# Performance work log

Measured on AMD Instinct MI355X. Metric: run time of the kernel, lower is better.

## Reference

```python
import jax, jax.numpy as jnp
import numpy as np

NUM_QUESTION = 10000


def setup_inputs() -> dict:
    key = jax.random.key(0)
    ks = jax.random.split(key, 12)
    B, L, DK, SLOTS = 64, 200, 128, 64
    return {
        "question_seq": jax.random.randint(ks[0], (B, L), 0, NUM_QUESTION),
        "correct_seq": jax.random.randint(ks[1], (B, L), 0, 2),
        "q_emb": jax.random.normal(ks[2], (NUM_QUESTION, DK), jnp.float32) * 0.05,
        "v_emb": jax.random.normal(ks[3], (2 * NUM_QUESTION, DK), jnp.float32) * 0.05,
        "Mk": jax.random.normal(ks[4], (SLOTS, DK), jnp.float32) * 0.1,
        "Mv0": jax.random.normal(ks[5], (SLOTS, DK), jnp.float32) * 0.1,
        "eW": jax.random.normal(ks[6], (DK, DK), jnp.float32) * 0.05,
        "eb": jnp.zeros((DK,), jnp.float32),
        "aW": jax.random.normal(ks[7], (DK, DK), jnp.float32) * 0.05,
        "ab": jnp.zeros((DK,), jnp.float32),
        "fW": jax.random.normal(ks[8], (DK, 2 * DK), jnp.float32) * 0.05,
        "fb": jnp.zeros((DK,), jnp.float32),
        "pW": jax.random.normal(ks[9], (1, DK), jnp.float32) * 0.05,
        "pb": jnp.zeros((1,), jnp.float32),
    }


def reference(question_seq, correct_seq, q_emb, v_emb, Mk, Mv0,
              eW, eb, aW, ab, fW, fb, pW, pb):
    B = question_seq.shape[0]
    x = question_seq + NUM_QUESTION * correct_seq          # [B, L]
    k = q_emb[question_seq]                                # [B, L, DK]
    v = v_emb[x]                                           # [B, L, DK]
    w = jax.nn.softmax(jnp.einsum("bld,sd->bls", k, Mk), axis=-1)  # [B, L, S]
    e = jax.nn.sigmoid(v @ eW.T + eb)                      # [B, L, DK]
    a = jnp.tanh(v @ aW.T + ab)                            # [B, L, DK]

    Mv_init = jnp.broadcast_to(Mv0[None], (B,) + Mv0.shape)  # [B, S, DK]

    def step(Mvt, inp):
        wt, et, at = inp  # [B,S], [B,DK], [B,DK]
        # read uses memory BEFORE the write (Mv[:, :-1] in the original)
        read = jnp.einsum("bs,bsd->bd", wt, Mvt)
        we = wt[:, :, None]
        Mvt = Mvt * (1.0 - we * et[:, None, :]) + we * at[:, None, :]
        return Mvt, read

    xs = (w.transpose(1, 0, 2), e.transpose(1, 0, 2), a.transpose(1, 0, 2))
    _, reads = jax.lax.scan(step, Mv_init, xs)             # reads: [L, B, DK]
    reads = reads.transpose(1, 0, 2)                       # [B, L, DK]

    f = jnp.tanh(jnp.concatenate([reads, k], axis=-1) @ fW.T + fb)
    predict_score = jax.nn.sigmoid(f @ pW.T + pb)[..., 0]  # [B, L]
    return predict_score
```

## Files before the change

### kernel.cpp

```cpp
#include <hip/hip_runtime.h>
#include <hip/hip_bf16.h>

#define NQ 10000
#define BATCH 64
#define SEQL 200
#define DKD 128
#define SLOTS 64
#define NTOK (BATCH*SEQL)

typedef __attribute__((ext_vector_type(8))) short bh8;
typedef __attribute__((ext_vector_type(4))) float f32x4;
typedef unsigned short u16;
typedef unsigned int u32;

__device__ __forceinline__ float sigmoidf_(float x){ return 1.0f/(1.0f + __expf(-x)); }
__device__ __forceinline__ float tanhf_(float x){
  float ax = fminf(fabsf(x), 30.0f);
  float t = __expf(-2.0f*ax);
  float r = (1.0f-t)/(1.0f+t);
  return copysignf(r, x);
}
__device__ __forceinline__ u16 f2b(float x){
  u32 u = __builtin_bit_cast(u32, x);
  u32 r = (u + 0x7FFFu + ((u >> 16) & 1u)) >> 16;
  return (u16)r;
}
__device__ __forceinline__ bh8 cvt8(const float* s){
  float4 v0 = *(const float4*)s, v1 = *(const float4*)(s + 4);
  bh8 h;
  h[0]=(short)f2b(v0.x); h[1]=(short)f2b(v0.y); h[2]=(short)f2b(v0.z); h[3]=(short)f2b(v0.w);
  h[4]=(short)f2b(v1.x); h[5]=(short)f2b(v1.y); h[6]=(short)f2b(v1.z); h[7]=(short)f2b(v1.w);
  return h;
}
__device__ __forceinline__ int swz(int row, int col16, int rowBytes){
  return row*rowBytes + ((col16 ^ (row & 7)) << 4);
}

__global__ __launch_bounds__(512) void wea_kernel(
    const int* __restrict__ qseq, const int* __restrict__ cseq,
    const float* __restrict__ q_emb, const float* __restrict__ v_emb,
    const float* __restrict__ Mk, const float* __restrict__ eW,
    const float* __restrict__ aW,
    const float* __restrict__ eb, const float* __restrict__ ab,
    float* __restrict__ w_out, float* __restrict__ eT, float* __restrict__ aT)
{
  __shared__ __align__(16) char smem[73728];
  char* As = smem;
  char* Bs = smem + 8192;
  float* Ls = (float*)(smem + 24576);

  const int tid = threadIdx.x;
  const int l = tid & 63, wv = tid >> 6;
  const bool isW = (blockIdx.x < 400);
  const int tok0 = (isW ? blockIdx.x : blockIdx.x - 400) * 32;

  {
    int row = tid >> 4, c16 = tid & 15;
    const float* src;
    if (isW){ int q = qseq[tok0+row]; src = q_emb + (size_t)q*DKD + c16*8; }
    else    { int x = qseq[tok0+row] + NQ*cseq[tok0+row]; src = v_emb + (size_t)x*DKD + c16*8; }
    *(bh8*)(As + swz(row, c16, 256)) = cvt8(src);
  }
  if (isW){
    #pragma unroll
    for (int m = 0; m < 2; ++m){
      int idx = tid + 512*m; int row = idx >> 4, c16 = idx & 15;
      *(bh8*)(Bs + swz(row, c16, 256)) = cvt8(Mk + (size_t)row*DKD + c16*8);
    }
  } else {
    #pragma unroll
    for (int m = 0; m < 8; ++m){
      int idx = tid + 512*m; int row = idx >> 4, c16 = idx & 15;
      const float* src = (row < 128) ? (eW + (size_t)row*DKD) : (aW + (size_t)(row-128)*DKD);
      *(bh8*)(Bs + swz(row, c16, 256)) = cvt8(src + c16*8);
    }
  }
  __syncthreads();

  if (isW){
    const int m = wv & 1, n = wv >> 1;
    f32x4 acc = {0.f,0.f,0.f,0.f};
    #pragma unroll
    for (int kc = 0; kc < 4; ++kc){
      bh8 af = *(const bh8*)(As + swz(m*16 + (l&15), kc*4 + (l>>4), 256));
      bh8 bf = *(const bh8*)(Bs + swz(n*16 + (l&15), kc*4 + (l>>4), 256));
      acc = __builtin_amdgcn_mfma_f32_16x16x32_bf16(af, bf, acc, 0, 0, 0);
    }
    #pragma unroll
    for (int r = 0; r < 4; ++r){
      int tok = m*16 + (l>>4)*4 + r, out = n*16 + (l&15);
      Ls[tok*68 + out] = acc[r];
    }
    __syncthreads();
    #pragma unroll
    for (int i = 0; i < 4; ++i){
      int tok = wv*4 + i;
      float x = Ls[tok*68 + l];
      float mx = x;
      #pragma unroll
      for (int off = 32; off >= 1; off >>= 1) mx = fmaxf(mx, __shfl_xor(mx, off));
      float p = __expf(x - mx);
      float s = p;
      #pragma unroll
      for (int off = 32; off >= 1; off >>= 1) s += __shfl_xor(s, off);
      w_out[(size_t)(tok0+tok)*SLOTS + l] = p / s;
    }
  } else {
    const int m = wv & 1, nq = (wv >> 1) * 4;
    f32x4 acc[4] = {{0.f,0.f,0.f,0.f},{0.f,0.f,0.f,0.f},{0.f,0.f,0.f,0.f},{0.f,0.f,0.f,0.f}};
    #pragma unroll
    for (int kc = 0; kc < 4; ++kc){
      bh8 af = *(const bh8*)(As + swz(m*16 + (l&15), kc*4 + (l>>4), 256));
      #pragma unroll
      for (int j = 0; j < 4; ++j){
        bh8 bf = *(const bh8*)(Bs + swz((nq+j)*16 + (l&15), kc*4 + (l>>4), 256));
        acc[j] = __builtin_amdgcn_mfma_f32_16x16x32_bf16(af, bf, acc[j], 0, 0, 0);
      }
    }
    #pragma unroll
    for (int j = 0; j < 4; ++j){
      int out = (nq+j)*16 + (l&15);
      bool is_e = (out < 128);
      int dd = out & 127;
      float bias = is_e ? eb[dd] : ab[dd];
      f32x4 sv;
      #pragma unroll
      for (int r = 0; r < 4; ++r){
        float xv = acc[j][r] + bias;
        sv[r] = is_e ? sigmoidf_(xv) : tanhf_(xv);
      }
      int tg = tok0 + m*16 + (l>>4)*4;
      int bb = tg / SEQL, tl = tg - bb*SEQL;
      float* dst = (is_e ? eT : aT) + ((size_t)bb*DKD + dd)*SEQL + tl;
      *(f32x4*)dst = sv;
    }
  }
}

__device__ __forceinline__ float dpp_row_sum16(float x){
  float t;
  t = __builtin_bit_cast(float, __builtin_amdgcn_update_dpp(0, __builtin_bit_cast(int,x), 0x111, 0xf, 0xf, true)); x += t;
  t = __builtin_bit_cast(float, __builtin_amdgcn_update_dpp(0, __builtin_bit_cast(int,x), 0x112, 0xf, 0xf, true)); x += t;
  t = __builtin_bit_cast(float, __builtin_amdgcn_update_dpp(0, __builtin_bit_cast(int,x), 0x114, 0xf, 0xf, true)); x += t;
  t = __builtin_bit_cast(float, __builtin_amdgcn_update_dpp(0, __builtin_bit_cast(int,x), 0x118, 0xf, 0xf, true)); x += t;
  return x;
}

#define TCH 8

__global__ __launch_bounds__(256) void scan_kernel(
    const float* __restrict__ Mv0,
    const float* __restrict__ w_in,
    const float* __restrict__ eT,
    const float* __restrict__ aT,
    u16* __restrict__ r16)
{
  __shared__ float eS[16][204];
  __shared__ float aS[16][204];
  const int tid = threadIdx.x;
  const int bid = blockIdx.x;
  const int b   = bid & 63;
  const int d0  = (bid >> 6) << 4;
  const int c   = tid >> 4;
  const int g   = tid & 15;
  const int d   = d0 + c;
  const bool wl = (g == 15);

  #pragma unroll
  for (int m = 0; m < 7; ++m){
    int i = tid + 256*m;
    if (i < 1600){
      int arr = (i >= 800);
      int j = arr ? i - 800 : i;
      int row = j / 50, col = j - row*50;
      const float* src = (arr ? aT : eT) + ((size_t)b*DKD + d0 + row)*SEQL + col*4;
      float4 v = *(const float4*)src;
      float* dst = (arr ? &aS[0][0] : &eS[0][0]) + row*204 + col*4;
      *(float4*)dst = v;
    }
  }

  float mv0 = Mv0[(4*g+0)*DKD + d];
  float mv1 = Mv0[(4*g+1)*DKD + d];
  float mv2 = Mv0[(4*g+2)*DKD + d];
  float mv3 = Mv0[(4*g+3)*DKD + d];

  const float* wsrc = w_in + (size_t)b*SEQL*SLOTS + 4*g;
  u16* rp = r16 + (size_t)b*SEQL*DKD + d;

  f32x4 Aw[TCH], Bw[TCH], Cw[TCH];

  #define LOADS(S, CK) { \
    _Pragma("unroll") \
    for (int i = 0; i < TCH; ++i) \
      S[i] = *(const f32x4*)(wsrc + (size_t)((CK)*TCH + i)*SLOTS); \
    asm volatile("" ::: "memory"); }

  #define CHUNK(S, CK) { \
    _Pragma("unroll") \
    for (int u = 0; u < 2; ++u){ \
      float eq[4], aq[4]; \
      *(float4*)eq = *(const float4*)&eS[c][(CK)*TCH + u*4]; \
      *(float4*)aq = *(const float4*)&aS[c][(CK)*TCH + u*4]; \
      _Pragma("unroll") \
      for (int v = 0; v < 4; ++v){ \
        const int tt = u*4 + v; \
        const float w0 = S[tt][0], w1 = S[tt][1], w2 = S[tt][2], w3 = S[tt][3]; \
        float r = w0*mv0; r = fmaf(w1, mv1, r); \
        r = fmaf(w2, mv2, r); r = fmaf(w3, mv3, r); \
        r = dpp_row_sum16(r); \
        if (wl) rp[(size_t)((CK)*TCH + tt)*DKD] = f2b(r); \
        const float ev = eq[v], av = aq[v]; \
        mv0 = fmaf(w0, fmaf(-mv0, ev, av), mv0); \
        mv1 = fmaf(w1, fmaf(-mv1, ev, av), mv1); \
        mv2 = fmaf(w2, fmaf(-mv2, ev, av), mv2); \
        mv3 = fmaf(w3, fmaf(-mv3, ev, av), mv3); \
      } \
    } }

  LOADS(Aw, 0)
  LOADS(Bw, 1)
  __syncthreads();

  #pragma unroll 1
  for (int m = 0; m < 7; ++m){
    const int ck = 3*m;
    LOADS(Cw, ck+2)  CHUNK(Aw, ck)
    LOADS(Aw, ck+3)  CHUNK(Bw, ck+1)
    LOADS(Bw, ck+4)  CHUNK(Cw, ck+2)
  }
  LOADS(Cw, 23)  CHUNK(Aw, 21)
  LOADS(Aw, 24)  CHUNK(Bw, 22)
  CHUNK(Cw, 23)
  CHUNK(Aw, 24)
  #undef LOADS
  #undef CHUNK
}

__global__ __launch_bounds__(512) void p3_kernel(
    const int* __restrict__ qseq, const float* __restrict__ q_emb,
    const u16* __restrict__ r16, const float* __restrict__ fW,
    const float* __restrict__ fb, const float* __restrict__ pW,
    const float* __restrict__ pb, float* __restrict__ out)
{
  __shared__ __align__(16) char smem[81920];
  char* As = smem;
  char* Bs = smem + 16384;

  const int tid = threadIdx.x;
  const int l = tid & 63, wv = tid >> 6;
  const int tok0 = blockIdx.x * 32;

  #pragma unroll
  for (int m = 0; m < 2; ++m){
    int idx = tid + 512*m; int row = idx >> 5, c16 = idx & 31;
    bh8 v;
    if (c16 < 16){
      v = *(const bh8*)(r16 + (size_t)(tok0+row)*DKD + c16*8);
    } else {
      int q = qseq[tok0+row];
      v = cvt8(q_emb + (size_t)q*DKD + (c16-16)*8);
    }
    *(bh8*)(As + swz(row, c16, 512)) = v;
  }
  #pragma unroll
  for (int m = 0; m < 8; ++m){
    int idx = tid + 512*m; int row = idx >> 5, c16 = idx & 31;
    *(bh8*)(Bs + swz(row, c16, 512)) = cvt8(fW + (size_t)row*256 + c16*8);
  }
  __syncthreads();

  const int m = wv & 1, np = (wv >> 1) * 2;
  f32x4 acc[2] = {{0.f,0.f,0.f,0.f},{0.f,0.f,0.f,0.f}};
  #pragma unroll
  for (int kc = 0; kc < 8; ++kc){
    bh8 af = *(const bh8*)(As + swz(m*16 + (l&15), kc*4 + (l>>4), 512));
    #pragma unroll
    for (int j = 0; j < 2; ++j){
      bh8 bf = *(const bh8*)(Bs + swz((np+j)*16 + (l&15), kc*4 + (l>>4), 512));
      acc[j] = __builtin_amdgcn_mfma_f32_16x16x32_bf16(af, bf, acc[j], 0, 0, 0);
    }
  }
  float pp[4] = {0.f,0.f,0.f,0.f};
  #pragma unroll
  for (int j = 0; j < 2; ++j){
    int o = (np+j)*16 + (l&15);
    float bias = fb[o], pw = pW[o];
    #pragma unroll
    for (int r = 0; r < 4; ++r){
      float f = tanhf_(acc[j][r] + bias);
      pp[r] = fmaf(f, pw, pp[r]);
    }
  }
  #pragma unroll
  for (int r = 0; r < 4; ++r){
    pp[r] += __shfl_xor(pp[r], 1);
    pp[r] += __shfl_xor(pp[r], 2);
    pp[r] += __shfl_xor(pp[r], 4);
    pp[r] += __shfl_xor(pp[r], 8);
  }
  __syncthreads();
  float* pbuf = (float*)smem;
  if ((l & 15) == 0){
    #pragma unroll
    for (int r = 0; r < 4; ++r){
      int tok = m*16 + (l>>4)*4 + r;
      pbuf[wv*32 + tok] = pp[r];
    }
  }
  __syncthreads();
  if (tid < 32){
    int mm = tid >> 4;
    float s = pbuf[(mm+0)*32 + tid] + pbuf[(mm+2)*32 + tid]
            + pbuf[(mm+4)*32 + tid] + pbuf[(mm+6)*32 + tid];
    out[tok0 + tid] = sigmoidf_(s + pb[0]);
  }
}

extern "C" void kernel_launch(void* const* d_in, const int* in_sizes, int n_in,
                              void* d_out, int out_size, void* d_ws, size_t ws_size,
                              hipStream_t stream) {
  const int*   qseq  = (const int*)d_in[0];
  const int*   cseq  = (const int*)d_in[1];
  const float* q_emb = (const float*)d_in[2];
  const float* v_emb = (const float*)d_in[3];
  const float* Mk    = (const float*)d_in[4];
  const float* Mv0   = (const float*)d_in[5];
  const float* eW    = (const float*)d_in[6];
  const float* eb    = (const float*)d_in[7];
  const float* aW    = (const float*)d_in[8];
  const float* ab    = (const float*)d_in[9];
  const float* fW    = (const float*)d_in[10];
  const float* fb    = (const float*)d_in[11];
  const float* pW    = (const float*)d_in[12];
  const float* pb    = (const float*)d_in[13];

  char* ws = (char*)d_ws;
  float* w_buf = (float*)ws;
  float* eT    = (float*)(ws + 3276800);
  float* aT    = (float*)(ws + 9830400);
  u16*   r16   = (u16*)  (ws + 16384000);
  float* outp  = (float*)d_out;

  hipLaunchKernelGGL(wea_kernel, dim3(800), dim3(512), 0, stream,
                     qseq, cseq, q_emb, v_emb, Mk, eW, aW, eb, ab,
                     w_buf, eT, aT);
  hipLaunchKernelGGL(scan_kernel, dim3(512), dim3(256), 0, stream,
                     Mv0, w_buf, eT, aT, r16);
  hipLaunchKernelGGL(p3_kernel, dim3(NTOK/32), dim3(512), 0, stream,
                     qseq, q_emb, r16, fW, fb, pW, pb, outp);
}
```

Before: 53.32 us.

## Remap scan to one wave per column with one slot per lane

The memory scan kernel is restructured so each wavefront owns one feature column and each lane owns one memory slot, instead of 16 lanes each holding four slots. The read is now reduced across the whole wave with DPP row-broadcast steps. The e/a sequences are read straight from global memory rather than staged through LDS. The grid grows fourfold to expose more independent waves for latency hiding, at the cost of a longer reduction chain per step and more redundant weight loads. The bf16 conversion now uses an inline v_cvt_pk_bf16_f32 instruction.

Measured after the change: 80.52 us. 1.51x slower.

```diff
diff --git a/kernel.cpp b/kernel.cpp
--- a/kernel.cpp
+++ b/kernel.cpp
@@ -137,104 +137,81 @@
   }
 }
 
-__device__ __forceinline__ float dpp_row_sum16(float x){
+__device__ __forceinline__ float wave_sum64(float x){
   float t;
-  t = __builtin_bit_cast(float, __builtin_amdgcn_update_dpp(0, __builtin_bit_cast(int,x), 0x111, 0xf, 0xf, true)); x += t;
-  t = __builtin_bit_cast(float, __builtin_amdgcn_update_dpp(0, __builtin_bit_cast(int,x), 0x112, 0xf, 0xf, true)); x += t;
-  t = __builtin_bit_cast(float, __builtin_amdgcn_update_dpp(0, __builtin_bit_cast(int,x), 0x114, 0xf, 0xf, true)); x += t;
-  t = __builtin_bit_cast(float, __builtin_amdgcn_update_dpp(0, __builtin_bit_cast(int,x), 0x118, 0xf, 0xf, true)); x += t;
+  #define DPPADD(ctrl) \
+    t = __builtin_bit_cast(float, __builtin_amdgcn_update_dpp(0, __builtin_bit_cast(int,x), ctrl, 0xf, 0xf, true)); x += t;
+  DPPADD(0x111)
+  DPPADD(0x112)
+  DPPADD(0x114)
+  DPPADD(0x118)
+  DPPADD(0x142)
+  DPPADD(0x143)
+  #undef DPPADD
   return x;
 }
 
-#define TCH 8
-
-__global__ __launch_bounds__(256) void scan_kernel(
+__global__ __launch_bounds__(256, 8) void scan_kernel(
     const float* __restrict__ Mv0,
     const float* __restrict__ w_in,
     const float* __restrict__ eT,
     const float* __restrict__ aT,
     u16* __restrict__ r16)
 {
-  __shared__ float eS[16][204];
-  __shared__ float aS[16][204];
   const int tid = threadIdx.x;
+  const int l  = tid & 63;
+  const int wv = tid >> 6;
   const int bid = blockIdx.x;
-  const int b   = bid & 63;
-  const int d0  = (bid >> 6) << 4;
-  const int c   = tid >> 4;
-  const int g   = tid & 15;
-  const int d   = d0 + c;
-  const bool wl = (g == 15);
-
-  #pragma unroll
-  for (int m = 0; m < 7; ++m){
-    int i = tid + 256*m;
-    if (i < 1600){
-      int arr = (i >= 800);
-      int j = arr ? i - 800 : i;
-      int row = j / 50, col = j - row*50;
-      const float* src = (arr ? aT : eT) + ((size_t)b*DKD + d0 + row)*SEQL + col*4;
-      float4 v = *(const float4*)src;
-      float* dst = (arr ? &aS[0][0] : &eS[0][0]) + row*204 + col*4;
-      *(float4*)dst = v;
-    }
-  }
-
-  float mv0 = Mv0[(4*g+0)*DKD + d];
-  float mv1 = Mv0[(4*g+1)*DKD + d];
-  float mv2 = Mv0[(4*g+2)*DKD + d];
-  float mv3 = Mv0[(4*g+3)*DKD + d];
-
-  const float* wsrc = w_in + (size_t)b*SEQL*SLOTS + 4*g;
-  u16* rp = r16 + (size_t)b*SEQL*DKD + d;
-
-  f32x4 Aw[TCH], Bw[TCH], Cw[TCH];
-
-  #define LOADS(S, CK) { \
+  const int b  = bid & 63;
+  const int d  = ((bid >> 6) << 2) + wv;
+  const bool sl = (l == 63);
+
+  float mv = Mv0[l*DKD + d];
+
+  const float* wq = w_in + (size_t)b*SEQL*SLOTS + l;
+  const float* eq = eT + ((size_t)b*DKD + d)*SEQL;
+  const float* aq = aT + ((size_t)b*DKD + d)*SEQL;
+  u16* rq = r16 + (size_t)b*SEQL*DKD + d;
+
+  float wa[8], wb[8];
+
+  #define LOADW(W, OFF) { \
     _Pragma("unroll") \
-    for (int i = 0; i < TCH; ++i) \
-      S[i] = *(const f32x4*)(wsrc + (size_t)((CK)*TCH + i)*SLOTS); \
+    for (int i = 0; i < 8; ++i) W[i] = wq[((OFF)+i)*SLOTS]; \
     asm volatile("" ::: "memory"); }
 
-  #define CHUNK(S, CK) { \
+  #define CHUNK8(W, OFF) { \
+    f32x4 E0 = *(const f32x4*)(eq + (OFF)); \
+    f32x4 E1 = *(const f32x4*)(eq + (OFF) + 4); \
+    f32x4 A0 = *(const f32x4*)(aq + (OFF)); \
+    f32x4 A1 = *(const f32x4*)(aq + (OFF) + 4); \
     _Pragma("unroll") \
-    for (int u = 0; u < 2; ++u){ \
-      float eq[4], aq[4]; \
-      *(float4*)eq = *(const float4*)&eS[c][(CK)*TCH + u*4]; \
-      *(float4*)aq = *(const float4*)&aS[c][(CK)*TCH + u*4]; \
-      _Pragma("unroll") \
-      for (int v = 0; v < 4; ++v){ \
-        const int tt = u*4 + v; \
-        const float w0 = S[tt][0], w1 = S[tt][1], w2 = S[tt][2], w3 = S[tt][3]; \
-        float r = w0*mv0; r = fmaf(w1, mv1, r); \
-        r = fmaf(w2, mv2, r); r = fmaf(w3, mv3, r); \
-        r = dpp_row_sum16(r); \
-        if (wl) rp[(size_t)((CK)*TCH + tt)*DKD] = f2b(r); \
-        const float ev = eq[v], av = aq[v]; \
-        mv0 = fmaf(w0, fmaf(-mv0, ev, av), mv0); \
-        mv1 = fmaf(w1, fmaf(-mv1, ev, av), mv1); \
-        mv2 = fmaf(w2, fmaf(-mv2, ev, av), mv2); \
-        mv3 = fmaf(w3, fmaf(-mv3, ev, av), mv3); \
+    for (int v = 0; v < 8; ++v){ \
+      const float ev = (v < 4) ? E0[v] : E1[v-4]; \
+      const float av = (v < 4) ? A0[v] : A1[v-4]; \
+      float r = W[v] * mv; \
+      r = wave_sum64(r); \
+      if (sl){ \
+        u32 pk; \
+        asm volatile("v_cvt_pk_bf16_f32 %0, %1, %2" : "=v"(pk) : "v"(r), "v"(0.f)); \
+        rq[v*DKD] = (u16)pk; \
       } \
-    } }
-
-  LOADS(Aw, 0)
-  LOADS(Bw, 1)
-  __syncthreads();
-
+      mv = fmaf(W[v], fmaf(-mv, ev, av), mv); \
+    } \
+    rq += 8*DKD; }
+
+  LOADW(wa, 0)
   #pragma unroll 1
-  for (int m = 0; m < 7; ++m){
-    const int ck = 3*m;
-    LOADS(Cw, ck+2)  CHUNK(Aw, ck)
-    LOADS(Aw, ck+3)  CHUNK(Bw, ck+1)
-    LOADS(Bw, ck+4)  CHUNK(Cw, ck+2)
-  }
-  LOADS(Cw, 23)  CHUNK(Aw, 21)
-  LOADS(Aw, 24)  CHUNK(Bw, 22)
-  CHUNK(Cw, 23)
-  CHUNK(Aw, 24)
-  #undef LOADS
-  #undef CHUNK
+  for (int m = 0; m < 12; ++m){
+    LOADW(wb, 8)
+    CHUNK8(wa, 0)
+    LOADW(wa, 16)
+    CHUNK8(wb, 8)
+    wq += 16*SLOTS; eq += 16; aq += 16;
+  }
+  CHUNK8(wa, 0)
+  #undef LOADW
+  #undef CHUNK8
 }
 
 __global__ __launch_bounds__(512) void p3_kernel(
@@ -345,7 +322,7 @@
   hipLaunchKernelGGL(wea_kernel, dim3(800), dim3(512), 0, stream,
                      qseq, cseq, q_emb, v_emb, Mk, eW, aW, eb, ab,
                      w_buf, eT, aT);
-  hipLaunchKernelGGL(scan_kernel, dim3(512), dim3(256), 0, stream,
+  hipLaunchKernelGGL(scan_kernel, dim3(2048), dim3(256), 0, stream,
                      Mv0, w_buf, eT, aT, r16);
   hipLaunchKernelGGL(p3_kernel, dim3(NTOK/32), dim3(512), 0, stream,
                      qseq, q_emb, r16, fW, fb, pW, pb, outp);
```

## Store softmax weights as bf16 and stage them in LDS for the scan

Applied to the files above, without the earlier changes.

The first kernel now writes the softmax slot weights as bf16 instead of fp32, halving the bytes written to and read back from the workspace. The scan kernel loads a batch's whole 200x64 weight tile into shared memory once, converting it back to fp32. The recurrent loop then reads weights from shared memory instead of through a triple-buffered register pipeline of global loads. This shortens the per-step load path and cuts global traffic, at the cost of a large LDS allocation per block and bf16 rounding of the attention weights.

Result: no change. 52.48 us (-1.6%).

```diff
diff --git a/kernel.cpp b/kernel.cpp
--- a/kernel.cpp
+++ b/kernel.cpp
@@ -25,6 +25,9 @@
   u32 r = (u + 0x7FFFu + ((u >> 16) & 1u)) >> 16;
   return (u16)r;
 }
+__device__ __forceinline__ float b2f(u16 h){
+  return __builtin_bit_cast(float, (u32)h << 16);
+}
 __device__ __forceinline__ bh8 cvt8(const float* s){
   float4 v0 = *(const float4*)s, v1 = *(const float4*)(s + 4);
   bh8 h;
@@ -42,7 +45,7 @@
     const float* __restrict__ Mk, const float* __restrict__ eW,
     const float* __restrict__ aW,
     const float* __restrict__ eb, const float* __restrict__ ab,
-    float* __restrict__ w_out, float* __restrict__ eT, float* __restrict__ aT)
+    u16* __restrict__ w16, float* __restrict__ eT, float* __restrict__ aT)
 {
   __shared__ __align__(16) char smem[73728];
   char* As = smem;
@@ -103,7 +106,7 @@
       float s = p;
       #pragma unroll
       for (int off = 32; off >= 1; off >>= 1) s += __shfl_xor(s, off);
-      w_out[(size_t)(tok0+tok)*SLOTS + l] = p / s;
+      w16[(size_t)(tok0+tok)*SLOTS + l] = f2b(p / s);
     }
   } else {
     const int m = wv & 1, nq = (wv >> 1) * 4;
@@ -146,15 +149,14 @@
   return x;
 }
 
-#define TCH 8
-
 __global__ __launch_bounds__(256) void scan_kernel(
     const float* __restrict__ Mv0,
-    const float* __restrict__ w_in,
+    const u16* __restrict__ w16,
     const float* __restrict__ eT,
     const float* __restrict__ aT,
     u16* __restrict__ r16)
 {
+  __shared__ float wS[200][68];
   __shared__ float eS[16][204];
   __shared__ float aS[16][204];
   const int tid = threadIdx.x;
@@ -170,6 +172,22 @@
   for (int m = 0; m < 7; ++m){
     int i = tid + 256*m;
     if (i < 1600){
+      int t8 = i & 7, blk = i >> 3;
+      int c8 = i / 200;
+      int tt = i - c8*200;
+      const u16* src = w16 + (size_t)b*SEQL*SLOTS + (size_t)tt*SLOTS + c8*8;
+      bh8 v = *(const bh8*)src;
+      float f[8];
+      #pragma unroll
+      for (int j = 0; j < 8; ++j) f[j] = b2f((u16)v[j]);
+      *(float4*)&wS[tt][c8*8]     = *(const float4*)&f[0];
+      *(float4*)&wS[tt][c8*8 + 4] = *(const float4*)&f[4];
+    }
+  }
+  #pragma unroll
+  for (int m = 0; m < 7; ++m){
+    int i = tid + 256*m;
+    if (i < 1600){
       int arr = (i >= 800);
       int j = arr ? i - 800 : i;
       int row = j / 50, col = j - row*50;
@@ -184,57 +202,33 @@
   float mv1 = Mv0[(4*g+1)*DKD + d];
   float mv2 = Mv0[(4*g+2)*DKD + d];
   float mv3 = Mv0[(4*g+3)*DKD + d];
-
-  const float* wsrc = w_in + (size_t)b*SEQL*SLOTS + 4*g;
-  u16* rp = r16 + (size_t)b*SEQL*DKD + d;
-
-  f32x4 Aw[TCH], Bw[TCH], Cw[TCH];
-
-  #define LOADS(S, CK) { \
-    _Pragma("unroll") \
-    for (int i = 0; i < TCH; ++i) \
-      S[i] = *(const f32x4*)(wsrc + (size_t)((CK)*TCH + i)*SLOTS); \
-    asm volatile("" ::: "memory"); }
-
-  #define CHUNK(S, CK) { \
-    _Pragma("unroll") \
-    for (int u = 0; u < 2; ++u){ \
-      float eq[4], aq[4]; \
-      *(float4*)eq = *(const float4*)&eS[c][(CK)*TCH + u*4]; \
-      *(float4*)aq = *(const float4*)&aS[c][(CK)*TCH + u*4]; \
-      _Pragma("unroll") \
-      for (int v = 0; v < 4; ++v){ \
-        const int tt = u*4 + v; \
-        const float w0 = S[tt][0], w1 = S[tt][1], w2 = S[tt][2], w3 = S[tt][3]; \
-        float r = w0*mv0; r = fmaf(w1, mv1, r); \
-        r = fmaf(w2, mv2, r); r = fmaf(w3, mv3, r); \
-        r = dpp_row_sum16(r); \
-        if (wl) rp[(size_t)((CK)*TCH + tt)*DKD] = f2b(r); \
-        const float ev = eq[v], av = aq[v]; \
-        mv0 = fmaf(w0, fmaf(-mv0, ev, av), mv0); \
-        mv1 = fmaf(w1, fmaf(-mv1, ev, av), mv1); \
-        mv2 = fmaf(w2, fmaf(-mv2, ev, av), mv2); \
-        mv3 = fmaf(w3, fmaf(-mv3, ev, av), mv3); \
-      } \
-    } }
-
-  LOADS(Aw, 0)
-  LOADS(Bw, 1)
-  __syncthreads();
-
-  #pragma unroll 1
-  for (int m = 0; m < 7; ++m){
-    const int ck = 3*m;
-    LOADS(Cw, ck+2)  CHUNK(Aw, ck)
-    LOADS(Aw, ck+3)  CHUNK(Bw, ck+1)
-    LOADS(Bw, ck+4)  CHUNK(Cw, ck+2)
-  }
-  LOADS(Cw, 23)  CHUNK(Aw, 21)
-  LOADS(Aw, 24)  CHUNK(Bw, 22)
-  CHUNK(Cw, 23)
-  CHUNK(Aw, 24)
-  #undef LOADS
-  #undef CHUNK
+  u16* rq = r16 + (size_t)b*SEQL*DKD + d;
+
+  __syncthreads();
+
+  for (int ck = 0; ck < 25; ++ck){
+    const int t0 = ck*8;
+    #pragma unroll
+    for (int u = 0; u < 2; ++u){
+      float eq[4], aq[4];
+      *(float4*)eq = *(const float4*)&eS[c][t0 + u*4];
+      *(float4*)aq = *(const float4*)&aS[c][t0 + u*4];
+      #pragma unroll
+      for (int v = 0; v < 4; ++v){
+        const int tt = t0 + u*4 + v;
+        float4 wq = *(const float4*)&wS[tt][4*g];
+        float r = wq.x*mv0; r = fmaf(wq.y, mv1, r);
+        r = fmaf(wq.z, mv2, r); r = fmaf(wq.w, mv3, r);
+        r = dpp_row_sum16(r);
+        if (wl) rq[(size_t)tt*DKD] = f2b(r);
+        const float ev = eq[v], av = aq[v];
+        mv0 = fmaf(wq.x, fmaf(-mv0, ev, av), mv0);
+        mv1 = fmaf(wq.y, fmaf(-mv1, ev, av), mv1);
+        mv2 = fmaf(wq.z, fmaf(-mv2, ev, av), mv2);
+        mv3 = fmaf(wq.w, fmaf(-mv3, ev, av), mv3);
+      }
+    }
+  }
 }
 
 __global__ __launch_bounds__(512) void p3_kernel(
@@ -336,7 +330,7 @@
   const float* pb    = (const float*)d_in[13];
 
   char* ws = (char*)d_ws;
-  float* w_buf = (float*)ws;
+  u16*   w16   = (u16*)ws;
   float* eT    = (float*)(ws + 3276800);
   float* aT    = (float*)(ws + 9830400);
   u16*   r16   = (u16*)  (ws + 16384000);
@@ -344,9 +338,9 @@
 
   hipLaunchKernelGGL(wea_kernel, dim3(800), dim3(512), 0, stream,
                      qseq, cseq, q_emb, v_emb, Mk, eW, aW, eb, ab,
-                     w_buf, eT, aT);
+                     w16, eT, aT);
   hipLaunchKernelGGL(scan_kernel, dim3(512), dim3(256), 0, stream,
-                     Mv0, w_buf, eT, aT, r16);
+                     Mv0, w16, eT, aT, r16);
   hipLaunchKernelGGL(p3_kernel, dim3(NTOK/32), dim3(512), 0, stream,
                      qseq, q_emb, r16, fW, fb, pW, pb, outp);
 }
```
